# Kernel optimization log

Measured on AMD Instinct MI355X. Metric: run time of the kernel, lower is better.

## Reference

```python
import jax, jax.numpy as jnp
import numpy as np

B, T, D, H = 4, 2048, 1024, 8
HD = D // H  # head_dim = 128


def setup_inputs() -> dict:
    key = jax.random.key(0)
    ks = jax.random.split(key, 10)
    s = 1.0 / np.sqrt(D)
    return {
        "x": jax.random.normal(ks[0], (B, T, D), jnp.float32),
        "y": jax.random.normal(ks[1], (B, T, D), jnp.float32),
        "Wq": jax.random.normal(ks[2], (D, D), jnp.float32) * s,
        "bq": jnp.zeros((D,), jnp.float32),
        "Wk": jax.random.normal(ks[3], (D, D), jnp.float32) * s,
        "bk": jnp.zeros((D,), jnp.float32),
        "Wv": jax.random.normal(ks[4], (D, D), jnp.float32) * s,
        "bv": jnp.zeros((D,), jnp.float32),
        "Wo": jax.random.normal(ks[5], (D, D), jnp.float32) * s,
        "bo": jnp.zeros((D,), jnp.float32),
    }


def _heads(t):
    # [B, T, D] -> [B, H, T, HD]
    b, t_, _ = t.shape
    return t.reshape(b, t_, H, HD).transpose(0, 2, 1, 3)


def reference(x, y, Wq, bq, Wk, bk, Wv, bv, Wo, bo):
    Tq, Tk = x.shape[1], y.shape[1]
    q = _heads(x @ Wq.T + bq)  # [B,H,Tq,HD]
    k = _heads(y @ Wk.T + bk)  # [B,H,Tk,HD]
    v = _heads(y @ Wv.T + bv)  # [B,H,Tk,HD]
    scale = 1.0 / np.sqrt(HD)
    logits = jnp.einsum("bhqd,bhkd->bhqk", q, k) * scale
    # causal mask: positions k > q get -inf
    causal = jnp.triu(jnp.full((Tq, Tk), -jnp.inf, jnp.float32), k=1)
    logits = logits + causal
    attn = jax.nn.softmax(logits, axis=-1)  # [B,H,Tq,Tk]
    ctx = jnp.einsum("bhqk,bhkd->bhqd", attn, v)
    ctx = ctx.transpose(0, 2, 1, 3).reshape(x.shape[0], Tq, D)
    out = ctx @ Wo.T + bo
    return out
```

## Files before the change

### kernel.cpp

```cpp
#include <hip/hip_runtime.h>
#include <math.h>

#define TB 4
#define TT 2048
#define TD 1024
#define TH 8
#define THD 128

typedef __attribute__((ext_vector_type(8))) short short8;
typedef __attribute__((ext_vector_type(4))) short short4v;
typedef __attribute__((ext_vector_type(4))) float float4v;
typedef __attribute__((ext_vector_type(16))) float float16v;
typedef __attribute__((ext_vector_type(4))) unsigned uint4v;

__device__ __forceinline__ short f2bf(float f) {
    union { float f; unsigned u; } v; v.f = f;
    unsigned r = v.u + 0x7FFFu + ((v.u >> 16) & 1u);
    return (short)(r >> 16);
}

__device__ __forceinline__ float bf2f(short s) {
    union { unsigned u; float f; } v;
    v.u = ((unsigned)(unsigned short)s) << 16;
    return v.f;
}

__device__ __forceinline__ short8 cvt8(float4v a, float4v b) {
    short8 r;
    r[0] = f2bf(a[0]); r[1] = f2bf(a[1]); r[2] = f2bf(a[2]); r[3] = f2bf(a[3]);
    r[4] = f2bf(b[0]); r[5] = f2bf(b[1]); r[6] = f2bf(b[2]); r[7] = f2bf(b[3]);
    return r;
}

__device__ __forceinline__ void async16(const void* g, void* l) {
    __builtin_amdgcn_global_load_lds(
        (const __attribute__((address_space(1))) unsigned int*)g,
        (__attribute__((address_space(3))) unsigned int*)l, 16, 0, 0);
}

__global__ void cvtall(const float* __restrict__ x, const float* __restrict__ y,
                       const float* __restrict__ wq, const float* __restrict__ wk,
                       const float* __restrict__ wv, const float* __restrict__ wo,
                       short* __restrict__ xyb, short* __restrict__ wb)
{
    const size_t SZ = (size_t)TB * TT * TD;
    const size_t WSZ = (size_t)TD * TD;
    int ty = blockIdx.y;
    const float* s; short* d; size_t n;
    if (ty == 0)      { s = x;  d = xyb;      n = SZ; }
    else if (ty == 1) { s = y;  d = xyb + SZ; n = SZ; }
    else {
        s = (ty == 2) ? wq : (ty == 3) ? wk : (ty == 4) ? wv : wo;
        d = wb + (size_t)(ty - 2) * WSZ; n = WSZ;
    }
    size_t i = ((size_t)blockIdx.x * blockDim.x + threadIdx.x) * 8;
    if (i >= n) return;
    float4v v0 = *(const float4v*)(s + i);
    float4v v1 = *(const float4v*)(s + i + 4);
    *(short8*)(d + i) = cvt8(v0, v1);
}

__device__ __forceinline__ void gemm_core256(const short* __restrict__ A,
                                             const short* __restrict__ W,
                                             int m0, int n0, short* SM,
                                             float4v acc[4][4])
{
    short* As = SM;
    short* Bs = SM + 32768;
    const int tid = threadIdx.x;
    const int lane = tid & 63, wid = tid >> 6;
    const int lr = lane & 15, qd = lane >> 4, sw = lane & 7;
    const int wr = wid >> 1, wc = wid & 1;
    const int rsub = lane >> 3;
    const int gj = ((lane & 7) ^ rsub) * 8;
    const int K = TD;

    const short* aSrc[4]; int aDst[4];
    const short* bSrc[2]; int bDst[2];
#pragma unroll
    for (int p = 0; p < 4; ++p) {
        int ch = wid * 4 + p;
        aSrc[p] = A + (size_t)(m0 + ch * 8 + rsub) * K + gj;
        aDst[p] = ch * 512;
    }
#pragma unroll
    for (int p = 0; p < 2; ++p) {
        int ch = wid * 2 + p;
        bSrc[p] = W + (size_t)(n0 + ch * 8 + rsub) * K + gj;
        bDst[p] = ch * 512;
    }

#pragma unroll
    for (int mt = 0; mt < 4; ++mt)
#pragma unroll
        for (int nt = 0; nt < 4; ++nt)
            acc[mt][nt] = float4v{0.f, 0.f, 0.f, 0.f};

#pragma unroll
    for (int t = 0; t < 2; ++t) {
#pragma unroll
        for (int p = 0; p < 4; ++p)
            async16(aSrc[p] + t * 64, As + t * 16384 + aDst[p]);
#pragma unroll
        for (int p = 0; p < 2; ++p)
            async16(bSrc[p] + t * 64, Bs + t * 8192 + bDst[p]);
    }
    asm volatile("s_waitcnt vmcnt(6)" ::: "memory");
    __builtin_amdgcn_sched_barrier(0);
    __builtin_amdgcn_s_barrier();

#pragma unroll 2
    for (int it = 0; it < 16; ++it) {
        const short* Ac = As + (it & 1) * 16384;
        const short* Bc = Bs + (it & 1) * 8192;
        short* Asn = As + (it & 1) * 16384;
        short* Bsn = Bs + (it & 1) * 8192;
        const int kb2 = (it + 2) * 64;
        const bool stg = (it < 14);

        short8 af[4][2], bf[4][2];

#pragma unroll
        for (int mi = 0; mi < 4; ++mi)
#pragma unroll
            for (int ks = 0; ks < 2; ++ks)
                af[mi][ks] = *(const short8*)&Ac[(wr * 64 + mi * 16 + lr) * 64 +
                                                 (((ks * 4 + qd) ^ sw) * 8)];
#pragma unroll
        for (int ni = 0; ni < 2; ++ni)
#pragma unroll
            for (int ks = 0; ks < 2; ++ks)
                bf[ni][ks] = *(const short8*)&Bc[(wc * 64 + ni * 16 + lr) * 64 +
                                                 (((ks * 4 + qd) ^ sw) * 8)];
        __builtin_amdgcn_sched_barrier(0);
#pragma unroll
        for (int ni = 2; ni < 4; ++ni)
#pragma unroll
            for (int ks = 0; ks < 2; ++ks)
                bf[ni][ks] = *(const short8*)&Bc[(wc * 64 + ni * 16 + lr) * 64 +
                                                 (((ks * 4 + qd) ^ sw) * 8)];
        asm volatile("s_waitcnt lgkmcnt(4)" ::: "memory");
        __builtin_amdgcn_sched_barrier(0);
        __builtin_amdgcn_s_setprio(1);
#pragma unroll
        for (int mi = 0; mi < 4; ++mi)
#pragma unroll
            for (int ni = 0; ni < 2; ++ni)
#pragma unroll
                for (int ks = 0; ks < 2; ++ks)
                    acc[mi][ni] = __builtin_amdgcn_mfma_f32_16x16x32_bf16(
                        af[mi][ks], bf[ni][ks], acc[mi][ni], 0, 0, 0);
        __builtin_amdgcn_s_setprio(0);
        __builtin_amdgcn_sched_barrier(0);
        asm volatile("s_waitcnt lgkmcnt(0)" ::: "memory");
        __builtin_amdgcn_sched_barrier(0);
        __builtin_amdgcn_s_barrier();
        __builtin_amdgcn_sched_barrier(0);

        if (stg) {
#pragma unroll
            for (int p = 0; p < 4; ++p)
                async16(aSrc[p] + kb2, Asn + aDst[p]);
#pragma unroll
            for (int p = 0; p < 2; ++p)
                async16(bSrc[p] + kb2, Bsn + bDst[p]);
        }
        __builtin_amdgcn_s_setprio(1);
#pragma unroll
        for (int mi = 0; mi < 4; ++mi)
#pragma unroll
            for (int ni = 2; ni < 4; ++ni)
#pragma unroll
                for (int ks = 0; ks < 2; ++ks)
                    acc[mi][ni] = __builtin_amdgcn_mfma_f32_16x16x32_bf16(
                        af[mi][ks], bf[ni][ks], acc[mi][ni], 0, 0, 0);
        __builtin_amdgcn_s_setprio(0);
        if (stg) { asm volatile("s_waitcnt vmcnt(6)" ::: "memory"); }
        else     { asm volatile("s_waitcnt vmcnt(0)" ::: "memory"); }
        __builtin_amdgcn_sched_barrier(0);
        __builtin_amdgcn_s_barrier();
    }
}

__global__ __launch_bounds__(512, 2)
void gemm_qkv8(const short* __restrict__ xyb, const short* __restrict__ wb,
               const float* __restrict__ bq, const float* __restrict__ bk,
               const float* __restrict__ bv,
               short* __restrict__ qhp, short* __restrict__ khp,
               short* __restrict__ vtp)
{
    __shared__ __attribute__((aligned(16))) short SM[49152];
    const size_t SZ = (size_t)TB * TT * TD;
    const int bid = blockIdx.x;
    const int lin = (bid & 7) * 96 + (bid >> 3);
    const int by = lin / 24, bx = lin - by * 24;
    const int mode = bx >> 3;
    const int n0 = (bx & 7) * 128;
    const int h_ = n0 >> 7;
    const int m0 = by * 256;
    const short* A = (mode == 0) ? xyb : (xyb + SZ);
    const short* W = wb + (size_t)mode * TD * TD;
    const float* bias = (mode == 0) ? bq : (mode == 1) ? bk : bv;
    const float scale = (mode == 0)
        ? (0.08838834764831845f * 1.4426950408889634f) : 1.0f;

    float4v acc[4][4];
    gemm_core256(A, W, m0, n0, SM, acc);

    const int tid = threadIdx.x;
    const int lane = tid & 63, wid = tid >> 6;
    const int lr = lane & 15, qd = lane >> 4;
    const int wr = wid >> 1, wc = wid & 1;

#pragma unroll
    for (int nt = 0; nt < 4; ++nt) {
        int col = wc * 64 + nt * 16 + lr;
        float bi = bias[n0 + col];
#pragma unroll
        for (int mt = 0; mt < 4; ++mt)
#pragma unroll
            for (int i = 0; i < 4; ++i) {
                int row = wr * 64 + mt * 16 + qd * 4 + i;
                short v = f2bf((acc[mt][nt][i] + bi) * scale);
                if (mode < 2) SM[row * 128 + col] = v;
                else          SM[col * 264 + row] = v;
            }
    }
    __syncthreads();

    if (mode < 2) {
        short* outp = (mode == 0) ? qhp : khp;
#pragma unroll
        for (int r8 = 0; r8 < 8; ++r8) {
            int row = r8 * 32 + (tid >> 4), c = tid & 15;
            short8 v = *(const short8*)&SM[row * 128 + c * 8];
            int tg = m0 + row;
            int b_ = tg >> 11, t_ = tg & (TT - 1);
            *(short8*)&outp[(((size_t)(b_ * TH + h_)) * TT + t_) * THD + c * 8] = v;
        }
    } else {
        int b_ = m0 >> 11, t0 = m0 & (TT - 1);
#pragma unroll
        for (int r8 = 0; r8 < 8; ++r8) {
            int hd = r8 * 16 + (tid >> 5), c = tid & 31;
            short8 v = *(const short8*)&SM[hd * 264 + c * 8];
            *(short8*)&vtp[(((size_t)(b_ * TH + h_)) * THD + hd) * TT + t0 + c * 8] = v;
        }
    }
}

__global__ __launch_bounds__(512, 2)
void gemm_out8(const short* __restrict__ A, const short* __restrict__ W,
               const float* __restrict__ bias, float* __restrict__ outp)
{
    __shared__ __attribute__((aligned(16))) short SM[49152];
    const int bid = blockIdx.x;
    const int lin = (bid & 7) * 32 + (bid >> 3);
    const int by = lin >> 3, bx = lin & 7;
    const int m0 = by * 256, n0 = bx * 128;

    float4v acc[4][4];
    gemm_core256(A, W, m0, n0, SM, acc);

    const int tid = threadIdx.x;
    const int lane = tid & 63, wid = tid >> 6;
    const int lr = lane & 15, qd = lane >> 4;
    const int wr = wid >> 1, wc = wid & 1;
#pragma unroll
    for (int nt = 0; nt < 4; ++nt) {
        int col = n0 + wc * 64 + nt * 16 + lr;
        float bi = bias[col];
#pragma unroll
        for (int mt = 0; mt < 4; ++mt)
#pragma unroll
            for (int i = 0; i < 4; ++i) {
                int row = m0 + wr * 64 + mt * 16 + qd * 4 + i;
                outp[(size_t)row * TD + col] = acc[mt][nt][i] + bi;
            }
    }
}

__global__ __launch_bounds__(256, 2)
void attn_fwd(const short* __restrict__ qh, const short* __restrict__ kh,
              const short* __restrict__ vt, short* __restrict__ po,
              float* __restrict__ pl)
{
    __shared__ __attribute__((aligned(16))) short Ks[2][64 * 128];
    __shared__ __attribute__((aligned(16))) short Vs[2][128 * 64];

    const int tid = threadIdx.x;
    const int lane = tid & 63, wid = tid >> 6;
    const int l31 = lane & 31, h = lane >> 5;
    const int sw7 = l31 & 7;
    const int sw15 = l31 & 15;

    const int bi = blockIdx.x;
    const int bh = bi & 31;
    const int j  = bi >> 5;
    const size_t bho = (size_t)bh * TT * THD;

    for (int u = 0; u < 2; ++u) {
        const int qt  = u ? (15 - j) : j;
        const int kv0 = u ? (qt + 1) : 0;
        const int kv1 = u ? (2 * qt + 2) : (j + 1);

        short8 qf[8];
        {
            const short* qp = qh + bho + (size_t)(qt * 128 + wid * 32 + l31) * THD;
#pragma unroll
            for (int ks = 0; ks < 8; ++ks)
                qf[ks] = *(const short8*)(qp + ks * 16 + h * 8);
        }
        float16v o[4];
#pragma unroll
        for (int db = 0; db < 4; ++db)
#pragma unroll
            for (int r = 0; r < 16; ++r) o[db][r] = 0.f;
        float li = 0.f;

        {
            const short* kbase = kh + bho + (size_t)kv0 * 64 * THD;
            const short* vbase = vt + (size_t)bh * THD * TT + (size_t)kv0 * 64;
#pragma unroll
            for (int p = 0; p < 4; ++p) {
                int ch = wid * 4 + p;
                int kr = ch * 4 + (lane >> 4);
                int kg = (lane & 15) ^ (kr & 15);
                async16(kbase + (size_t)kr * THD + kg * 8, &Ks[0][ch * 512]);
                int vr = ch * 8 + (lane >> 3);
                int vg = (lane & 7) ^ (vr & 7);
                async16(vbase + (size_t)vr * TT + vg * 8, &Vs[0][ch * 512]);
            }
        }
        __syncthreads();

        int cur = 0;
        for (int kv = kv0; kv < kv1; ++kv) {
            if (kv + 1 < kv1) {
                const short* kbase = kh + bho + (size_t)(kv + 1) * 64 * THD;
                const short* vbase = vt + (size_t)bh * THD * TT +
                                     (size_t)(kv + 1) * 64;
#pragma unroll
                for (int p = 0; p < 4; ++p) {
                    int ch = wid * 4 + p;
                    int kr = ch * 4 + (lane >> 4);
                    int kg = (lane & 15) ^ (kr & 15);
                    async16(kbase + (size_t)kr * THD + kg * 8,
                            &Ks[cur ^ 1][ch * 512]);
                    int vr = ch * 8 + (lane >> 3);
                    int vg = (lane & 7) ^ (vr & 7);
                    async16(vbase + (size_t)vr * TT + vg * 8,
                            &Vs[cur ^ 1][ch * 512]);
                }
            }

            const short* Kc = Ks[cur];
            const short* Vc = Vs[cur];

            float16v s[2];
#pragma unroll
            for (int kb = 0; kb < 2; ++kb)
#pragma unroll
                for (int r = 0; r < 16; ++r) s[kb][r] = 0.f;
#pragma unroll
            for (int ks = 0; ks < 8; ++ks) {
                int cidx = ((ks * 2 + h) ^ sw15) * 8;
                short8 kf0 = *(const short8*)&Kc[l31 * 128 + cidx];
                short8 kf1 = *(const short8*)&Kc[(32 + l31) * 128 + cidx];
                s[0] = __builtin_amdgcn_mfma_f32_32x32x16_bf16(kf0, qf[ks], s[0], 0, 0, 0);
                s[1] = __builtin_amdgcn_mfma_f32_32x32x16_bf16(kf1, qf[ks], s[1], 0, 0, 0);
            }

            if (kv >= 2 * qt) {
                int q = qt * 128 + wid * 32 + l31;
#pragma unroll
                for (int r = 0; r < 16; ++r) {
                    int key = kv * 64 + (r & 3) + 8 * (r >> 2) + 4 * h;
                    if (key > q) s[0][r] = -1e30f;
                    if (key + 32 > q) s[1][r] = -1e30f;
                }
            }

#pragma unroll
            for (int t = 0; t < 4; ++t) {
                const int rA = ((2 * t) & 3) * 4, rB = ((2 * t + 1) & 3) * 4;
                const int kb = t >> 1;
                float eA0 = exp2f(s[kb][rA + 0]), eA1 = exp2f(s[kb][rA + 1]);
                float eA2 = exp2f(s[kb][rA + 2]), eA3 = exp2f(s[kb][rA + 3]);
                float eB0 = exp2f(s[kb][rB + 0]), eB1 = exp2f(s[kb][rB + 1]);
                float eB2 = exp2f(s[kb][rB + 2]), eB3 = exp2f(s[kb][rB + 3]);
                li += ((eA0 + eA1) + (eA2 + eA3)) + ((eB0 + eB1) + (eB2 + eB3));
                unsigned a0, a1, b0, b1;
                asm("v_cvt_pk_bf16_f32 %0, %1, %2" : "=v"(a0) : "v"(eA0), "v"(eA1));
                asm("v_cvt_pk_bf16_f32 %0, %1, %2" : "=v"(a1) : "v"(eA2), "v"(eA3));
                asm("v_cvt_pk_bf16_f32 %0, %1, %2" : "=v"(b0) : "v"(eB0), "v"(eB1));
                asm("v_cvt_pk_bf16_f32 %0, %1, %2" : "=v"(b1) : "v"(eB2), "v"(eB3));
                asm("v_permlane32_swap_b32 %0, %1" : "+v"(a0), "+v"(b0));
                asm("v_permlane32_swap_b32 %0, %1" : "+v"(a1), "+v"(b1));
                union { uint4v u; short8 s8; } pc;
                pc.u[0] = a0; pc.u[1] = a1; pc.u[2] = b0; pc.u[3] = b1;
                const short8 pa = pc.s8;
#pragma unroll
                for (int db = 0; db < 4; ++db) {
                    short8 vf = *(const short8*)&Vc[(db * 32 + l31) * 64 +
                                                    (((2 * t + h) ^ sw7) * 8)];
                    o[db] = __builtin_amdgcn_mfma_f32_32x32x16_bf16(
                        pa, vf, o[db], 0, 0, 0);
                }
            }
            __syncthreads();
            cur ^= 1;
        }

        li += __shfl_xor(li, 32);
        const int slot = (bh * 16 + qt) * 2 + u;
        if (h == 0) pl[slot * 128 + wid * 32 + l31] = li;
        short* pop = po + (size_t)slot * 16384 + (size_t)(wid * 32) * 128 + l31;
#pragma unroll
        for (int r = 0; r < 16; ++r) {
            int ql = (r & 3) + 8 * (r >> 2) + 4 * h;
#pragma unroll
            for (int db = 0; db < 4; ++db)
                pop[(size_t)ql * 128 + db * 32] = f2bf(o[db][r]);
        }
    }
}

__global__ __launch_bounds__(256)
void combine(const short* __restrict__ po, const float* __restrict__ pl,
             short* __restrict__ ctx)
{
    const unsigned i = blockIdx.x * 256 + threadIdx.x;
    const int hdv = i & 15;
    const int q   = (i >> 4) & 127;
    const int qt  = (i >> 11) & 15;
    const int bh  = i >> 15;
    const int tile = bh * 16 + qt;
    const size_t base = (size_t)tile * 2 * 16384 + (size_t)q * 128 + hdv * 8;
    short8 a = *(const short8*)&po[base];
    short8 b = *(const short8*)&po[base + 16384];
    const float inv = 1.f / (pl[tile * 2 * 128 + q] + pl[(tile * 2 + 1) * 128 + q]);
    short8 r;
#pragma unroll
    for (int k = 0; k < 8; ++k)
        r[k] = f2bf((bf2f(a[k]) + bf2f(b[k])) * inv);
    const int b_ = bh >> 3, h_ = bh & 7, t = qt * 128 + q;
    *(short8*)&ctx[((size_t)(b_ * TT + t)) * TD + h_ * THD + hdv * 8] = r;
}

extern "C" void kernel_launch(void* const* d_in, const int* in_sizes, int n_in,
                              void* d_out, int out_size, void* d_ws, size_t ws_size,
                              hipStream_t stream) {
    (void)in_sizes; (void)n_in; (void)out_size; (void)ws_size;
    const float* x  = (const float*)d_in[0];
    const float* y  = (const float*)d_in[1];
    const float* Wq = (const float*)d_in[2];
    const float* bq = (const float*)d_in[3];
    const float* Wk = (const float*)d_in[4];
    const float* bk = (const float*)d_in[5];
    const float* Wv = (const float*)d_in[6];
    const float* bv = (const float*)d_in[7];
    const float* Wo = (const float*)d_in[8];
    const float* bo = (const float*)d_in[9];
    float* out = (float*)d_out;

    const size_t SZ = (size_t)TB * TT * TD;
    const size_t WSZ = (size_t)TD * TD;
    short* xyb = (short*)d_ws;
    short* wb  = xyb + 2 * SZ;
    short* qh  = wb + 4 * WSZ;
    short* kh  = qh + SZ;
    short* vt  = kh + SZ;
    float* pl  = (float*)(vt + SZ);
    short* po  = xyb;
    short* ctx = qh;

    hipLaunchKernelGGL(cvtall, dim3(SZ / 2048, 6), dim3(256), 0, stream,
                       x, y, Wq, Wk, Wv, Wo, xyb, wb);
    hipLaunchKernelGGL(gemm_qkv8, dim3(768), dim3(512), 0, stream,
                       xyb, wb, bq, bk, bv, qh, kh, vt);
    hipLaunchKernelGGL(attn_fwd, dim3(512), dim3(256), 0, stream, qh, kh, vt, po, pl);
    hipLaunchKernelGGL(combine, dim3(4096), dim3(256), 0, stream, po, pl, ctx);
    hipLaunchKernelGGL(gemm_out8, dim3(256), dim3(512), 0, stream,
                       ctx, wb + 3 * WSZ, bo, out);
}
```

Baseline: 281.3 us.

## Use 256x256 output tiles for the fused QKV projection GEMM

Adds a new GEMM core that computes 256x256 tiles, with each wave owning a 128x64 sub-tile and an 8x4 accumulator array. The QKV kernel now launches half as many blocks, and its epilogue writes two head slices per block in two passes through shared memory. The larger tile raises arithmetic intensity and reuse of the A and B operands loaded into LDS. In exchange it uses more registers and 128KB of LDS per block, which may lower occupancy below the requested two blocks per CU, and it leaves fewer blocks to balance across the CUs.

```diff
diff --git a/kernel.cpp b/kernel.cpp
--- a/kernel.cpp
+++ b/kernel.cpp
@@ -60,6 +60,216 @@
     *(short8*)(d + i) = cvt8(v0, v1);
 }
 
+__device__ __forceinline__ void gemm_core256sq(const short* __restrict__ A,
+                                               const short* __restrict__ W,
+                                               int m0, int n0, short* SM,
+                                               float4v acc[8][4])
+{
+    short* As = SM;
+    short* Bs = SM + 32768;
+    const int tid = threadIdx.x;
+    const int lane = tid & 63, wid = tid >> 6;
+    const int lr = lane & 15, qd = lane >> 4, sw = lane & 7;
+    const int wr = wid >> 2, wc = wid & 3;
+    const int rsub = lane >> 3;
+    const int gj = ((lane & 7) ^ rsub) * 8;
+    const int K = TD;
+
+    const short* aSrc[4]; int aDst[4];
+    const short* bSrc[4]; int bDst[4];
+#pragma unroll
+    for (int p = 0; p < 4; ++p) {
+        int ch = wid * 4 + p;
+        aSrc[p] = A + (size_t)(m0 + ch * 8 + rsub) * K + gj;
+        aDst[p] = ch * 512;
+        bSrc[p] = W + (size_t)(n0 + ch * 8 + rsub) * K + gj;
+        bDst[p] = ch * 512;
+    }
+
+#pragma unroll
+    for (int mt = 0; mt < 8; ++mt)
+#pragma unroll
+        for (int nt = 0; nt < 4; ++nt)
+            acc[mt][nt] = float4v{0.f, 0.f, 0.f, 0.f};
+
+#pragma unroll
+    for (int t = 0; t < 2; ++t) {
+#pragma unroll
+        for (int p = 0; p < 4; ++p) {
+            async16(aSrc[p] + t * 64, As + t * 16384 + aDst[p]);
+            async16(bSrc[p] + t * 64, Bs + t * 16384 + bDst[p]);
+        }
+    }
+    asm volatile("s_waitcnt vmcnt(8)" ::: "memory");
+    __builtin_amdgcn_sched_barrier(0);
+    __builtin_amdgcn_s_barrier();
+
+#pragma unroll 2
+    for (int it = 0; it < 16; ++it) {
+        const short* Ac = As + (it & 1) * 16384;
+        const short* Bc = Bs + (it & 1) * 16384;
+        short* Asn = As + (it & 1) * 16384;
+        short* Bsn = Bs + (it & 1) * 16384;
+        const int kb2 = (it + 2) * 64;
+        const bool stg = (it < 14);
+
+        short8 af[8][2], bf[4][2];
+
+#pragma unroll
+        for (int mi = 0; mi < 4; ++mi)
+#pragma unroll
+            for (int ks = 0; ks < 2; ++ks)
+                af[mi][ks] = *(const short8*)&Ac[(wr * 128 + mi * 16 + lr) * 64 +
+                                                 (((ks * 4 + qd) ^ sw) * 8)];
+#pragma unroll
+        for (int ni = 0; ni < 4; ++ni)
+#pragma unroll
+            for (int ks = 0; ks < 2; ++ks)
+                bf[ni][ks] = *(const short8*)&Bc[(wc * 64 + ni * 16 + lr) * 64 +
+                                                 (((ks * 4 + qd) ^ sw) * 8)];
+        __builtin_amdgcn_sched_barrier(0);
+#pragma unroll
+        for (int mi = 4; mi < 8; ++mi)
+#pragma unroll
+            for (int ks = 0; ks < 2; ++ks)
+                af[mi][ks] = *(const short8*)&Ac[(wr * 128 + mi * 16 + lr) * 64 +
+                                                 (((ks * 4 + qd) ^ sw) * 8)];
+        asm volatile("s_waitcnt lgkmcnt(8)" ::: "memory");
+        __builtin_amdgcn_sched_barrier(0);
+        __builtin_amdgcn_s_setprio(1);
+#pragma unroll
+        for (int mi = 0; mi < 4; ++mi)
+#pragma unroll
+            for (int ni = 0; ni < 4; ++ni)
+#pragma unroll
+                for (int ks = 0; ks < 2; ++ks)
+                    acc[mi][ni] = __builtin_amdgcn_mfma_f32_16x16x32_bf16(
+                        af[mi][ks], bf[ni][ks], acc[mi][ni], 0, 0, 0);
+        __builtin_amdgcn_s_setprio(0);
+        __builtin_amdgcn_sched_barrier(0);
+        asm volatile("s_waitcnt lgkmcnt(0)" ::: "memory");
+        __builtin_amdgcn_sched_barrier(0);
+        __builtin_amdgcn_s_barrier();
+        __builtin_amdgcn_sched_barrier(0);
+
+        if (stg) {
+#pragma unroll
+            for (int p = 0; p < 4; ++p) {
+                async16(aSrc[p] + kb2, Asn + aDst[p]);
+                async16(bSrc[p] + kb2, Bsn + bDst[p]);
+            }
+        }
+        __builtin_amdgcn_s_setprio(1);
+#pragma unroll
+        for (int mi = 4; mi < 8; ++mi)
+#pragma unroll
+            for (int ni = 0; ni < 4; ++ni)
+#pragma unroll
+                for (int ks = 0; ks < 2; ++ks)
+                    acc[mi][ni] = __builtin_amdgcn_mfma_f32_16x16x32_bf16(
+                        af[mi][ks], bf[ni][ks], acc[mi][ni], 0, 0, 0);
+        __builtin_amdgcn_s_setprio(0);
+        if (stg) { asm volatile("s_waitcnt vmcnt(8)" ::: "memory"); }
+        else     { asm volatile("s_waitcnt vmcnt(0)" ::: "memory"); }
+        __builtin_amdgcn_sched_barrier(0);
+        __builtin_amdgcn_s_barrier();
+    }
+}
+
+__global__ __launch_bounds__(512, 2)
+void gemm_qkv8(const short* __restrict__ xyb, const short* __restrict__ wb,
+               const float* __restrict__ bq, const float* __restrict__ bk,
+               const float* __restrict__ bv,
+               short* __restrict__ qhp, short* __restrict__ khp,
+               short* __restrict__ vtp)
+{
+    __shared__ __attribute__((aligned(16))) short SM[65536];
+    const size_t SZ = (size_t)TB * TT * TD;
+    const int bid = blockIdx.x;
+    const int lin = (bid & 7) * 48 + (bid >> 3);
+    const int by = lin / 12, bxn = lin - by * 12;
+    const int mode = bxn >> 2;
+    const int n0 = (bxn & 3) * 256;
+    const int m0 = by * 256;
+    const short* A = (mode == 0) ? xyb : (xyb + SZ);
+    const short* W = wb + (size_t)mode * TD * TD;
+    const float* bias = (mode == 0) ? bq : (mode == 1) ? bk : bv;
+    const float scale = (mode == 0)
+        ? (0.08838834764831845f * 1.4426950408889634f) : 1.0f;
+
+    float4v acc[8][4];
+    gemm_core256sq(A, W, m0, n0, SM, acc);
+
+    const int tid = threadIdx.x;
+    const int lane = tid & 63, wid = tid >> 6;
+    const int lr = lane & 15, qd = lane >> 4;
+    const int wr = wid >> 2, wc = wid & 3;
+    const int b_ = m0 >> 11, t0 = m0 & (TT - 1);
+
+    if (mode < 2) {
+        short* outp = (mode == 0) ? qhp : khp;
+#pragma unroll
+        for (int hp = 0; hp < 2; ++hp) {
+            if (wr == hp) {
+#pragma unroll
+                for (int nt = 0; nt < 4; ++nt) {
+                    int col = wc * 64 + nt * 16 + lr;
+                    float bi = bias[n0 + col];
+#pragma unroll
+                    for (int mt = 0; mt < 8; ++mt)
+#pragma unroll
+                        for (int i = 0; i < 4; ++i) {
+                            int row128 = mt * 16 + qd * 4 + i;
+                            SM[row128 * 264 + col] =
+                                f2bf((acc[mt][nt][i] + bi) * scale);
+                        }
+                }
+            }
+            __syncthreads();
+#pragma unroll
+            for (int r8 = 0; r8 < 8; ++r8) {
+                int chunk = r8 * 512 + tid;
+                int row128 = chunk >> 5, c8 = chunk & 31;
+                short8 v = *(const short8*)&SM[row128 * 264 + c8 * 8];
+                int t_ = t0 + hp * 128 + row128;
+                int h_ = (n0 >> 7) + (c8 >> 4);
+                int hd = (c8 & 15) * 8;
+                *(short8*)&outp[(((size_t)(b_ * TH + h_)) * TT + t_) * THD + hd] = v;
+            }
+            __syncthreads();
+        }
+    } else {
+#pragma unroll
+        for (int hp = 0; hp < 2; ++hp) {
+            if ((wc >> 1) == hp) {
+#pragma unroll
+                for (int nt = 0; nt < 4; ++nt) {
+                    int col128 = (wc & 1) * 64 + nt * 16 + lr;
+                    float bi = bias[n0 + hp * 128 + col128];
+#pragma unroll
+                    for (int mt = 0; mt < 8; ++mt)
+#pragma unroll
+                        for (int i = 0; i < 4; ++i) {
+                            int row = wr * 128 + mt * 16 + qd * 4 + i;
+                            SM[col128 * 264 + row] = f2bf(acc[mt][nt][i] + bi);
+                        }
+                }
+            }
+            __syncthreads();
+            int h_ = (n0 >> 7) + hp;
+#pragma unroll
+            for (int r8 = 0; r8 < 8; ++r8) {
+                int chunk = r8 * 512 + tid;
+                int hd = chunk >> 5, tc = (chunk & 31) * 8;
+                short8 v = *(const short8*)&SM[hd * 264 + tc];
+                *(short8*)&vtp[(((size_t)(b_ * TH + h_)) * THD + hd) * TT +
+                               t0 + tc] = v;
+            }
+            __syncthreads();
+        }
+    }
+}
+
 __device__ __forceinline__ void gemm_core256(const short* __restrict__ A,
                                              const short* __restrict__ W,
                                              int m0, int n0, short* SM,
@@ -119,7 +329,6 @@
         const bool stg = (it < 14);
 
         short8 af[4][2], bf[4][2];
-
 #pragma unroll
         for (int mi = 0; mi < 4; ++mi)
 #pragma unroll
@@ -183,84 +392,17 @@
 }
 
 __global__ __launch_bounds__(512, 2)
-void gemm_qkv8(const short* __restrict__ xyb, const short* __restrict__ wb,
-               const float* __restrict__ bq, const float* __restrict__ bk,
-               const float* __restrict__ bv,
-               short* __restrict__ qhp, short* __restrict__ khp,
-               short* __restrict__ vtp)
-{
-    __shared__ __attribute__((aligned(16))) short SM[49152];
-    const size_t SZ = (size_t)TB * TT * TD;
-    const int bid = blockIdx.x;
-    const int lin = (bid & 7) * 96 + (bid >> 3);
-    const int by = lin / 24, bx = lin - by * 24;
-    const int mode = bx >> 3;
-    const int n0 = (bx & 7) * 128;
-    const int h_ = n0 >> 7;
-    const int m0 = by * 256;
-    const short* A = (mode == 0) ? xyb : (xyb + SZ);
-    const short* W = wb + (size_t)mode * TD * TD;
-    const float* bias = (mode == 0) ? bq : (mode == 1) ? bk : bv;
-    const float scale = (mode == 0)
-        ? (0.08838834764831845f * 1.4426950408889634f) : 1.0f;
-
-    float4v acc[4][4];
-    gemm_core256(A, W, m0, n0, SM, acc);
-
-    const int tid = threadIdx.x;
-    const int lane = tid & 63, wid = tid >> 6;
-    const int lr = lane & 15, qd = lane >> 4;
-    const int wr = wid >> 1, wc = wid & 1;
-
-#pragma unroll
-    for (int nt = 0; nt < 4; ++nt) {
-        int col = wc * 64 + nt * 16 + lr;
-        float bi = bias[n0 + col];
-#pragma unroll
-        for (int mt = 0; mt < 4; ++mt)
-#pragma unroll
-            for (int i = 0; i < 4; ++i) {
-                int row = wr * 64 + mt * 16 + qd * 4 + i;
-                short v = f2bf((acc[mt][nt][i] + bi) * scale);
-                if (mode < 2) SM[row * 128 + col] = v;
-                else          SM[col * 264 + row] = v;
-            }
-    }
-    __syncthreads();
-
-    if (mode < 2) {
-        short* outp = (mode == 0) ? qhp : khp;
-#pragma unroll
-        for (int r8 = 0; r8 < 8; ++r8) {
-            int row = r8 * 32 + (tid >> 4), c = tid & 15;
-            short8 v = *(const short8*)&SM[row * 128 + c * 8];
-            int tg = m0 + row;
-            int b_ = tg >> 11, t_ = tg & (TT - 1);
-            *(short8*)&outp[(((size_t)(b_ * TH + h_)) * TT + t_) * THD + c * 8] = v;
-        }
-    } else {
-        int b_ = m0 >> 11, t0 = m0 & (TT - 1);
-#pragma unroll
-        for (int r8 = 0; r8 < 8; ++r8) {
-            int hd = r8 * 16 + (tid >> 5), c = tid & 31;
-            short8 v = *(const short8*)&SM[hd * 264 + c * 8];
-            *(short8*)&vtp[(((size_t)(b_ * TH + h_)) * THD + hd) * TT + t0 + c * 8] = v;
-        }
-    }
-}
-
-__global__ __launch_bounds__(512, 2)
 void gemm_out8(const short* __restrict__ A, const short* __restrict__ W,
                const float* __restrict__ bias, float* __restrict__ outp)
 {
-    __shared__ __attribute__((aligned(16))) short SM[49152];
+    __shared__ __attribute__((aligned(16))) short SMo[49152];
     const int bid = blockIdx.x;
     const int lin = (bid & 7) * 32 + (bid >> 3);
     const int by = lin >> 3, bx = lin & 7;
     const int m0 = by * 256, n0 = bx * 128;
 
     float4v acc[4][4];
-    gemm_core256(A, W, m0, n0, SM, acc);
+    gemm_core256(A, W, m0, n0, SMo, acc);
 
     const int tid = threadIdx.x;
     const int lane = tid & 63, wid = tid >> 6;
@@ -477,7 +619,7 @@
 
     hipLaunchKernelGGL(cvtall, dim3(SZ / 2048, 6), dim3(256), 0, stream,
                        x, y, Wq, Wk, Wv, Wo, xyb, wb);
-    hipLaunchKernelGGL(gemm_qkv8, dim3(768), dim3(512), 0, stream,
+    hipLaunchKernelGGL(gemm_qkv8, dim3(384), dim3(512), 0, stream,
                        xyb, wb, bq, bk, bv, qh, kh, vt);
     hipLaunchKernelGGL(attn_fwd, dim3(512), dim3(256), 0, stream, qh, kh, vt, po, pl);
     hipLaunchKernelGGL(combine, dim3(4096), dim3(256), 0, stream, po, pl, ctx);
```

Result: slower. 354.5 us (+26.0%).
